# Kernel tuning notes

Measured on AMD Instinct MI355X. Metric: run time of the kernel, lower is better.

The kernel has to match this reference:

```python
import jax, jax.numpy as jnp
import numpy as np

N = 20000
E = 640000

def spmm(rows, cols, vals, x):
    # sparse [N,N] @ dense [N,D] via gather + segment-sum scatter
    return jax.ops.segment_sum(vals[:, None] * x[cols], rows, num_segments=N)

def setup_inputs() -> dict:
    key = jax.random.key(0)
    k1, k2, k3, k4, k5, k6 = jax.random.split(key, 6)
    feat = jax.random.normal(k1, (N, 512), dtype=jnp.float32)
    adj_rows = jax.random.randint(k2, (E,), 0, N, dtype=jnp.int32)
    adj_cols = jax.random.randint(k3, (E,), 0, N, dtype=jnp.int32)
    adj_vals = jax.random.uniform(k4, (E,), dtype=jnp.float32)
    # Xavier-uniform scaled weights
    lim1 = float(np.sqrt(6.0 / (512 + 256)))
    lim2 = float(np.sqrt(6.0 / (256 + 64)))
    W1 = jax.random.uniform(k5, (512, 256), minval=-lim1, maxval=lim1, dtype=jnp.float32)
    W2 = jax.random.uniform(k6, (256, 64), minval=-lim2, maxval=lim2, dtype=jnp.float32)
    return {"feat": feat, "adj_rows": adj_rows, "adj_cols": adj_cols,
            "adj_vals": adj_vals, "W1": W1, "W2": W2}

def reference(feat, adj_rows, adj_cols, adj_vals, W1, W2):
    # layer 1: dense GEMM then sparse aggregation (add_act=False, dropout=0)
    x = feat @ W1                      # [N, hid]
    x = spmm(adj_rows, adj_cols, adj_vals, x)
    # layer 2
    x = x @ W2                         # [N, out]
    z = spmm(adj_rows, adj_cols, adj_vals, x)
    # inner-product decoder (dropout=0 in module construction)
    A_rec = jax.nn.sigmoid(z @ z.T)    # [N, N]
    return (z, A_rec)
```

## Files before the change

kernel.cpp:

```cpp
#include <hip/hip_runtime.h>
#include <hip/hip_bf16.h>

#define NN 20000
#define EE 640000


typedef float f32x4 __attribute__((ext_vector_type(4)));
typedef short short8 __attribute__((ext_vector_type(8)));

__device__ __forceinline__ float sigf(float x) {
    return __builtin_amdgcn_rcpf(1.0f + __builtin_amdgcn_exp2f(x * -1.442695041f));
}

__global__ void fill_zero_i32(int* __restrict__ p, int n) {
    int i = blockIdx.x * 256 + threadIdx.x;
    if (i < n) p[i] = 0;
}

__global__ void count_rows(const int* __restrict__ rows, int* __restrict__ cnt, int e) {
    int i = blockIdx.x * 256 + threadIdx.x;
    if (i < e) atomicAdd(&cnt[rows[i]], 1);
}

__global__ __launch_bounds__(1024) void scan_counts(const int* __restrict__ cnt,
                                                    int* __restrict__ off,
                                                    int* __restrict__ cursor, int n) {
    __shared__ int part[1024];
    int tid = threadIdx.x;
    const int per = (n + 1023) / 1024;
    int base = tid * per;
    int s = 0;
    for (int i = 0; i < per; ++i) {
        int idx = base + i;
        if (idx < n) s += cnt[idx];
    }
    part[tid] = s;
    __syncthreads();
    for (int d = 1; d < 1024; d <<= 1) {
        int v = (tid >= d) ? part[tid - d] : 0;
        __syncthreads();
        part[tid] += v;
        __syncthreads();
    }
    int run = (tid == 0) ? 0 : part[tid - 1];
    for (int i = 0; i < per; ++i) {
        int idx = base + i;
        if (idx < n) {
            off[idx] = run;
            cursor[idx] = run;
            run += cnt[idx];
        }
    }
    if (tid == 1023) off[n] = part[1023];
}

__global__ void scatter_edges(const int* __restrict__ rows, const int* __restrict__ cols,
                              const float* __restrict__ vals, int* __restrict__ cursor,
                              int* __restrict__ col_s, float* __restrict__ val_s, int e) {
    int i = blockIdx.x * 256 + threadIdx.x;
    if (i < e) {
        int p = atomicAdd(&cursor[rows[i]], 1);
        col_s[p] = cols[i];
        val_s[p] = vals[i];
    }
}

__global__ __launch_bounds__(256) void sgemm64(const float* __restrict__ A,
                                               const float* __restrict__ B,
                                               float* __restrict__ C, int M, int K, int Nc) {
    __shared__ float As[16][65];
    __shared__ float Bs[16][65];
    int tid = threadIdx.x;
    int tm = (tid >> 4) << 2;
    int tn = (tid & 15) << 2;
    int m0 = blockIdx.y * 64;
    int n0 = blockIdx.x * 64;
    float acc[4][4] = {};
    for (int k0 = 0; k0 < K; k0 += 16) {
        for (int i = tid; i < 64 * 16; i += 256) {
            int r = i >> 4, c = i & 15;
            int gr = m0 + r;
            As[c][r] = (gr < M) ? A[(long)gr * K + k0 + c] : 0.0f;
        }
        for (int i = tid; i < 16 * 64; i += 256) {
            int kk = i >> 6, c = i & 63;
            Bs[kk][c] = B[(long)(k0 + kk) * Nc + n0 + c];
        }
        __syncthreads();
        #pragma unroll
        for (int kk = 0; kk < 16; ++kk) {
            float a[4], b[4];
            #pragma unroll
            for (int x = 0; x < 4; ++x) a[x] = As[kk][tm + x];
            #pragma unroll
            for (int y = 0; y < 4; ++y) b[y] = Bs[kk][tn + y];
            #pragma unroll
            for (int x = 0; x < 4; ++x)
                #pragma unroll
                for (int y = 0; y < 4; ++y)
                    acc[x][y] = fmaf(a[x], b[y], acc[x][y]);
        }
        __syncthreads();
    }
    for (int x = 0; x < 4; ++x) {
        int gr = m0 + tm + x;
        if (gr < M) {
            #pragma unroll
            for (int y = 0; y < 4; ++y) C[(long)gr * Nc + n0 + tn + y] = acc[x][y];
        }
    }
}

__global__ __launch_bounds__(256) void spmm_csr64(const int* __restrict__ off,
                                                  const int* __restrict__ col_s,
                                                  const float* __restrict__ val_s,
                                                  const float* __restrict__ X,
                                                  float* __restrict__ Y,
                                                  __hip_bfloat16* __restrict__ ZH,
                                                  __hip_bfloat16* __restrict__ ZL, int n) {
    int row = blockIdx.x * 4 + (threadIdx.x >> 6);
    if (row >= n) return;
    int lane = threadIdx.x & 63;
    int e0 = off[row], e1 = off[row + 1];
    float acc = 0.0f;
    for (int e = e0; e < e1; ++e) {
        acc = fmaf(val_s[e], X[(long)col_s[e] * 64 + lane], acc);
    }
    Y[(long)row * 64 + lane] = acc;
    if (ZH) {
        __hip_bfloat16 hi = __float2bfloat16(acc);
        __hip_bfloat16 lo = __float2bfloat16(acc - __bfloat162float(hi));
        ZH[(long)row * 64 + lane] = hi;
        ZL[(long)row * 64 + lane] = lo;
    }
}

__global__ __launch_bounds__(256, 2) void decoder_mfma(const __hip_bfloat16* __restrict__ ZH,
                                                       const __hip_bfloat16* __restrict__ ZL,
                                                       float* __restrict__ A, int n) {
    const short8* Zh8 = (const short8*)ZH;
    const short8* Zl8 = (const short8*)ZL;
    int tid = threadIdx.x;
    int lane = tid & 63;
    int wid = tid >> 6;
    int wrow = wid >> 1, wcol = wid & 1;
    int i0 = (blockIdx.y << 7) + (wrow << 6);
    int j0 = (blockIdx.x << 7) + (wcol << 6);
    int r16 = lane & 15;
    int kg = lane >> 4;

    f32x4 acc[4][4] = {};

    #pragma unroll
    for (int kc = 0; kc < 2; ++kc) {
        short8 ah[4], al[4], bh[4], bl[4];
        #pragma unroll
        for (int t = 0; t < 4; ++t) {
            int ra = i0 + t * 16 + r16; ra = (ra < n) ? ra : (n - 1);
            int rb = j0 + t * 16 + r16; rb = (rb < n) ? rb : (n - 1);
            long oa = (long)ra * 8 + kc * 4 + kg;
            long ob = (long)rb * 8 + kc * 4 + kg;
            ah[t] = Zh8[oa];
            al[t] = Zl8[oa];
            bh[t] = Zh8[ob];
            bl[t] = Zl8[ob];
        }
        #pragma unroll
        for (int ti = 0; ti < 4; ++ti)
            #pragma unroll
            for (int tj = 0; tj < 4; ++tj) {
                acc[ti][tj] = __builtin_amdgcn_mfma_f32_16x16x32_bf16(ah[ti], bh[tj], acc[ti][tj], 0, 0, 0);
                acc[ti][tj] = __builtin_amdgcn_mfma_f32_16x16x32_bf16(ah[ti], bl[tj], acc[ti][tj], 0, 0, 0);
                acc[ti][tj] = __builtin_amdgcn_mfma_f32_16x16x32_bf16(al[ti], bh[tj], acc[ti][tj], 0, 0, 0);
            }
    }

    #pragma unroll
    for (int ti = 0; ti < 4; ++ti) {
        int gib = i0 + ti * 16 + (kg << 2);
        #pragma unroll
        for (int q = 0; q < 4; ++q) {
            int gi = gib + q;
            if (gi < n) {
                long rowb = (long)gi * n;
                #pragma unroll
                for (int tj = 0; tj < 4; ++tj) {
                    int gj = j0 + tj * 16 + r16;
                    if (gj < n) A[rowb + gj] = sigf(acc[ti][tj][q]);
                }
            }
        }
    }
}

extern "C" void kernel_launch(void* const* d_in, const int* in_sizes, int n_in,
                              void* d_out, int out_size, void* d_ws, size_t ws_size,
                              hipStream_t stream) {
    const float* feat     = (const float*)d_in[0];
    const int*   adj_rows = (const int*)d_in[1];
    const int*   adj_cols = (const int*)d_in[2];
    const float* adj_vals = (const float*)d_in[3];
    const float* W1       = (const float*)d_in[4];
    const float* W2       = (const float*)d_in[5];

    float* out  = (float*)d_out;
    float* z    = out;
    float* Arec = out + (long)NN * 64;

    float* W12   = (float*)d_ws;
    float* h     = W12 + 512 * 64;
    float* hz    = h + (long)NN * 64;
    float* val_s = hz + (long)NN * 64;
    int*   col_s = (int*)(val_s + EE);
    int*   cnt   = col_s + EE;
    int*   off   = cnt + NN;
    int*   cursor= off + NN + 1;
    __hip_bfloat16* zh = (__hip_bfloat16*)h;
    __hip_bfloat16* zl = zh + (long)NN * 64;

    fill_zero_i32<<<(NN + 255) / 256, 256, 0, stream>>>(cnt, NN);
    count_rows<<<(EE + 255) / 256, 256, 0, stream>>>(adj_rows, cnt, EE);
    scan_counts<<<1, 1024, 0, stream>>>(cnt, off, cursor, NN);
    scatter_edges<<<(EE + 255) / 256, 256, 0, stream>>>(adj_rows, adj_cols, adj_vals,
                                                        cursor, col_s, val_s, EE);

    sgemm64<<<dim3(1, (512 + 63) / 64), 256, 0, stream>>>(W1, W2, W12, 512, 256, 64);
    sgemm64<<<dim3(1, (NN + 63) / 64), 256, 0, stream>>>(feat, W12, h, NN, 512, 64);

    spmm_csr64<<<(NN + 3) / 4, 256, 0, stream>>>(off, col_s, val_s, h, hz,
                                                 nullptr, nullptr, NN);
    spmm_csr64<<<(NN + 3) / 4, 256, 0, stream>>>(off, col_s, val_s, hz, z, zh, zl, NN);

    decoder_mfma<<<dim3((NN + 127) / 128, (NN + 127) / 128), 256, 0, stream>>>(zh, zl, Arec, NN);
}
```

Baseline: 2.095 ms.

## Exploit symmetry of z·zᵀ in decoder and split row counters to cut atomic contention

The decoder now computes only the lower-triangular block tiles and writes each tile twice, once directly and once transposed with float4 stores, which halves the MFMA work and the Z loads. The sigmoid is applied once per element before both stores. The CSR build also splits each row's counter into four sub-counters keyed by edge index, to reduce atomic contention in the count and scatter steps. These sub-counters live in the h buffer before the GEMM overwrites it. The transposed stores write scattered rows and may coalesce less well than the original row-major stores.

```diff
diff --git a/kernel.cpp b/kernel.cpp
--- a/kernel.cpp
+++ b/kernel.cpp
@@ -17,22 +17,22 @@
     if (i < n) p[i] = 0;
 }
 
-__global__ void count_rows(const int* __restrict__ rows, int* __restrict__ cnt, int e) {
+__global__ void count_rows(const int* __restrict__ rows, int* __restrict__ cnt4, int e) {
     int i = blockIdx.x * 256 + threadIdx.x;
-    if (i < e) atomicAdd(&cnt[rows[i]], 1);
-}
-
-__global__ __launch_bounds__(1024) void scan_counts(const int* __restrict__ cnt,
-                                                    int* __restrict__ off,
-                                                    int* __restrict__ cursor, int n) {
+    if (i < e) atomicAdd(&cnt4[(rows[i] << 2) | (i & 3)], 1);
+}
+
+__global__ __launch_bounds__(1024) void scan_counts4(const int* __restrict__ cnt4,
+                                                     int* __restrict__ off,
+                                                     int* __restrict__ cursor4, int n4) {
     __shared__ int part[1024];
     int tid = threadIdx.x;
-    const int per = (n + 1023) / 1024;
+    const int per = (n4 + 1023) / 1024;
     int base = tid * per;
     int s = 0;
     for (int i = 0; i < per; ++i) {
         int idx = base + i;
-        if (idx < n) s += cnt[idx];
+        if (idx < n4) s += cnt4[idx];
     }
     part[tid] = s;
     __syncthreads();
@@ -45,21 +45,21 @@
     int run = (tid == 0) ? 0 : part[tid - 1];
     for (int i = 0; i < per; ++i) {
         int idx = base + i;
-        if (idx < n) {
-            off[idx] = run;
-            cursor[idx] = run;
-            run += cnt[idx];
-        }
-    }
-    if (tid == 1023) off[n] = part[1023];
+        if (idx < n4) {
+            if ((idx & 3) == 0) off[idx >> 2] = run;
+            cursor4[idx] = run;
+            run += cnt4[idx];
+        }
+    }
+    if (tid == 1023) off[n4 >> 2] = part[1023];
 }
 
 __global__ void scatter_edges(const int* __restrict__ rows, const int* __restrict__ cols,
-                              const float* __restrict__ vals, int* __restrict__ cursor,
+                              const float* __restrict__ vals, int* __restrict__ cursor4,
                               int* __restrict__ col_s, float* __restrict__ val_s, int e) {
     int i = blockIdx.x * 256 + threadIdx.x;
     if (i < e) {
-        int p = atomicAdd(&cursor[rows[i]], 1);
+        int p = atomicAdd(&cursor4[(rows[i] << 2) | (i & 3)], 1);
         col_s[p] = cols[i];
         val_s[p] = vals[i];
     }
@@ -135,9 +135,10 @@
     }
 }
 
-__global__ __launch_bounds__(256, 2) void decoder_mfma(const __hip_bfloat16* __restrict__ ZH,
-                                                       const __hip_bfloat16* __restrict__ ZL,
-                                                       float* __restrict__ A, int n) {
+__global__ __launch_bounds__(256, 2) void decoder_mfma_sym(const __hip_bfloat16* __restrict__ ZH,
+                                                           const __hip_bfloat16* __restrict__ ZL,
+                                                           float* __restrict__ A, int n) {
+    if (blockIdx.x > blockIdx.y) return;
     const short8* Zh8 = (const short8*)ZH;
     const short8* Zl8 = (const short8*)ZL;
     int tid = threadIdx.x;
@@ -176,6 +177,14 @@
     }
 
     #pragma unroll
+    for (int ti = 0; ti < 4; ++ti)
+        #pragma unroll
+        for (int tj = 0; tj < 4; ++tj)
+            #pragma unroll
+            for (int q = 0; q < 4; ++q)
+                acc[ti][tj][q] = sigf(acc[ti][tj][q]);
+
+    #pragma unroll
     for (int ti = 0; ti < 4; ++ti) {
         int gib = i0 + ti * 16 + (kg << 2);
         #pragma unroll
@@ -186,7 +195,29 @@
                 #pragma unroll
                 for (int tj = 0; tj < 4; ++tj) {
                     int gj = j0 + tj * 16 + r16;
-                    if (gj < n) A[rowb + gj] = sigf(acc[ti][tj][q]);
+                    if (gj < n) A[rowb + gj] = acc[ti][tj][q];
+                }
+            }
+        }
+    }
+
+    if (blockIdx.x != blockIdx.y) {
+        #pragma unroll
+        for (int tj = 0; tj < 4; ++tj) {
+            int jr = j0 + tj * 16 + r16;
+            if (jr < n) {
+                long rowb = (long)jr * n;
+                #pragma unroll
+                for (int ti = 0; ti < 4; ++ti) {
+                    int c0 = i0 + ti * 16 + (kg << 2);
+                    if (c0 + 4 <= n) {
+                        float4 o;
+                        o.x = acc[ti][tj][0];
+                        o.y = acc[ti][tj][1];
+                        o.z = acc[ti][tj][2];
+                        o.w = acc[ti][tj][3];
+                        *(float4*)(A + rowb + c0) = o;
+                    }
                 }
             }
         }
@@ -212,17 +243,18 @@
     float* hz    = h + (long)NN * 64;
     float* val_s = hz + (long)NN * 64;
     int*   col_s = (int*)(val_s + EE);
-    int*   cnt   = col_s + EE;
-    int*   off   = cnt + NN;
-    int*   cursor= off + NN + 1;
+    int*   off   = col_s + EE;
+
+    int* cnt4    = (int*)h;
+    int* cursor4 = cnt4 + 4 * NN;
     __hip_bfloat16* zh = (__hip_bfloat16*)h;
     __hip_bfloat16* zl = zh + (long)NN * 64;
 
-    fill_zero_i32<<<(NN + 255) / 256, 256, 0, stream>>>(cnt, NN);
-    count_rows<<<(EE + 255) / 256, 256, 0, stream>>>(adj_rows, cnt, EE);
-    scan_counts<<<1, 1024, 0, stream>>>(cnt, off, cursor, NN);
+    fill_zero_i32<<<(4 * NN + 255) / 256, 256, 0, stream>>>(cnt4, 4 * NN);
+    count_rows<<<(EE + 255) / 256, 256, 0, stream>>>(adj_rows, cnt4, EE);
+    scan_counts4<<<1, 1024, 0, stream>>>(cnt4, off, cursor4, 4 * NN);
     scatter_edges<<<(EE + 255) / 256, 256, 0, stream>>>(adj_rows, adj_cols, adj_vals,
-                                                        cursor, col_s, val_s, EE);
+                                                        cursor4, col_s, val_s, EE);
 
     sgemm64<<<dim3(1, (512 + 63) / 64), 256, 0, stream>>>(W1, W2, W12, 512, 256, 64);
     sgemm64<<<dim3(1, (NN + 63) / 64), 256, 0, stream>>>(feat, W12, h, NN, 512, 64);
@@ -231,5 +263,5 @@
                                                  nullptr, nullptr, NN);
     spmm_csr64<<<(NN + 3) / 4, 256, 0, stream>>>(off, col_s, val_s, hz, z, zh, zl, NN);
 
-    decoder_mfma<<<dim3((NN + 127) / 128, (NN + 127) / 128), 256, 0, stream>>>(zh, zl, Arec, NN);
-}
+    decoder_mfma_sym<<<dim3((NN + 127) / 128, (NN + 127) / 128), 256, 0, stream>>>(zh, zl, Arec, NN);
+}
```

After: 2.191 ms. +4.6%, slower.
